# Kernel optimization log

Measured on AMD Instinct MI355X. Metric: run time of the kernel, lower is better.

## Reference

```python
import jax, jax.numpy as jnp
import numpy as np

N = 50000
E = 800000
IN_D, HID_D, EMB_D, K = 128, 128, 64, 16
ALPHA = 1.0
NEG_SLOPE = 0.2


def _l2norm(x, eps=1e-12):
    n = jnp.sqrt(jnp.sum(x * x, axis=1, keepdims=True))
    return x / jnp.maximum(n, eps)


def _gat(x, src, dst, W, a_src, a_dst, b, n_nodes):
    # PyG GATConv, heads=1: h = xW; e_ij = leakyrelu(a_src.h_j + a_dst.h_i)
    h = x @ W                                   # [N, D]
    al_s = h @ a_src                            # [N]
    al_d = h @ a_dst                            # [N]
    logits = jax.nn.leaky_relu(al_s[src] + al_d[dst], NEG_SLOPE)  # [E']
    m = jax.ops.segment_max(logits, dst, num_segments=n_nodes)
    ex = jnp.exp(logits - m[dst])
    denom = jax.ops.segment_sum(ex, dst, num_segments=n_nodes)
    alpha = ex / denom[dst]                     # softmax over incoming edges
    out = jax.ops.segment_sum(h[src] * alpha[:, None], dst, num_segments=n_nodes)
    return out + b


def _cluster_prob(z, cluster):
    z2 = jnp.sum(z * z, axis=1, keepdims=True)          # [N,1]
    c2 = jnp.sum(cluster * cluster, axis=1)[None, :]    # [1,K]
    dist = z2 + c2 - 2.0 * (z @ cluster.T)              # [N,K]
    q = 1.0 / (1.0 + dist / ALPHA)
    q = (q + 1e-07) ** ((ALPHA + 1.0) / 2.0)
    return q / jnp.sum(q, axis=1, keepdims=True)


def setup_inputs() -> dict:
    key = jax.random.key(0)
    ks = jax.random.split(key, 20)
    d = {}
    d['x'] = jax.random.normal(ks[0], (N, IN_D), dtype=jnp.float32)
    d['edge_index'] = jax.random.randint(ks[1], (2, E), 0, N, dtype=jnp.int32)
    dims = [(IN_D, HID_D), (HID_D, EMB_D), (EMB_D, HID_D), (HID_D, IN_D)]
    for i, (di, do) in enumerate(dims):
        s = 1.0 / np.sqrt(di)
        d[f'W{i+1}'] = jax.random.normal(ks[2 + 4 * i], (di, do), dtype=jnp.float32) * s
        d[f'a{i+1}s'] = jax.random.normal(ks[3 + 4 * i], (do,), dtype=jnp.float32) * 0.1
        d[f'a{i+1}d'] = jax.random.normal(ks[4 + 4 * i], (do,), dtype=jnp.float32) * 0.1
        d[f'b{i+1}'] = jnp.zeros((do,), dtype=jnp.float32)
    d['cluster'] = jax.random.normal(ks[18], (K, EMB_D), dtype=jnp.float32) * 0.1
    return d


def reference(x, edge_index, W1, a1s, a1d, b1, W2, a2s, a2d, b2,
              W3, a3s, a3d, b3, W4, a4s, a4d, b4, cluster):
    # add self loops (PyG GATConv default)
    loop = jnp.arange(N, dtype=edge_index.dtype)
    src = jnp.concatenate([edge_index[0], loop])
    dst = jnp.concatenate([edge_index[1], loop])

    xn = _l2norm(x)
    h1 = jax.nn.relu(_gat(xn, src, dst, W1, a1s, a1d, b1, N))
    z = _gat(h1, src, dst, W2, a2s, a2d, b2, N)
    z = _l2norm(z)
    d1 = jax.nn.relu(_gat(z, src, dst, W3, a3s, a3d, b3, N))
    x_hat = _gat(d1, src, dst, W4, a4s, a4d, b4, N)
    q = _cluster_prob(z, cluster)
    return (z, x_hat, q)
```

## Files before the change

### kernel.cpp

```cpp
#include <hip/hip_runtime.h>
#include <hip/hip_fp16.h>

#define NN 50000
#define NE 800000
#define NBK 196
#define BCAP 8192
#define GEMM_GRID 391
#define WTOT 49152

typedef unsigned int uint;
typedef unsigned short ushort;
typedef __attribute__((ext_vector_type(8))) short short8v;
typedef __attribute__((ext_vector_type(4))) float float4v;

static __device__ __forceinline__ float waveReduceSum(float v) {
#pragma unroll
  for (int o = 32; o > 0; o >>= 1) v += __shfl_xor(v, o);
  return v;
}
static __device__ __forceinline__ float waveReduceMax(float v) {
#pragma unroll
  for (int o = 32; o > 0; o >>= 1) v = fmaxf(v, __shfl_xor(v, o));
  return v;
}
static __device__ __forceinline__ uint f2bf(float f) {
  uint u = __float_as_uint(f);
  return (u + 0x7fffu + ((u >> 16) & 1u)) >> 16;
}
static __device__ __forceinline__ float h_lo(uint u) {
  __half2 h = *(const __half2*)&u;
  return __half2float(h.x);
}
static __device__ __forceinline__ float h_hi(uint u) {
  __half2 h = *(const __half2*)&u;
  return __half2float(h.y);
}
static __device__ __forceinline__ int waveInclScan(int v, int lane) {
#pragma unroll
  for (int o = 1; o < 64; o <<= 1) {
    int u = __shfl_up(v, o);
    if (lane >= o) v += u;
  }
  return v;
}
static __device__ __forceinline__ void split8(const float* f, short8v& hi, short8v& lo) {
#pragma unroll
  for (int j = 0; j < 8; ++j) {
    uint h = f2bf(f[j]);
    hi[j] = (short)h;
    float hf = __uint_as_float(h << 16);
    lo[j] = (short)f2bf(f[j] - hf);
  }
}

__global__ __launch_bounds__(256) void k_bucket(
    const int* __restrict__ esrc, const int* __restrict__ edst,
    uint* __restrict__ ebuf, int* __restrict__ bcnt) {
  __shared__ int hist[NBK];
  __shared__ int gbase[NBK];
  int tid = threadIdx.x;
  for (int i = tid; i < NBK; i += 256) hist[i] = 0;
  __syncthreads();
  const int ET = NE + NN;
  int base = blockIdx.x * 4096;
  int myb[16];
  uint mypk[16];
#pragma unroll
  for (int j = 0; j < 16; ++j) {
    int e = base + j * 256 + tid;
    int s, d;
    if (e < NE) { s = esrc[e]; d = edst[e]; }
    else if (e < ET) { s = e - NE; d = s; }
    else { myb[j] = -1; continue; }
    int b = d >> 8;
    myb[j] = b;
    mypk[j] = (uint)s | ((uint)(d & 255) << 16);
    atomicAdd(&hist[b], 1);
  }
  __syncthreads();
  for (int i = tid; i < NBK; i += 256) {
    int h = hist[i];
    gbase[i] = h > 0 ? atomicAdd(&bcnt[i], h) : 0;
    hist[i] = 0;
  }
  __syncthreads();
#pragma unroll
  for (int j = 0; j < 16; ++j) {
    int b = myb[j];
    if (b < 0) continue;
    int r = atomicAdd(&hist[b], 1);
    int pos = gbase[b] + r;
    if (pos < BCAP) ebuf[(size_t)b * BCAP + pos] = mypk[j];
  }
}
__global__ __launch_bounds__(256) void k_csr(
    const uint* __restrict__ ebuf, const int* __restrict__ bcnt,
    int* __restrict__ indptr, int* __restrict__ srcs) {
  __shared__ int h[256];
  __shared__ int cur[256];
  __shared__ int wsm[4];
  __shared__ int bbs;
  int tid = threadIdx.x, b = blockIdx.x;
  int lane = tid & 63, wv = tid >> 6;
  int v = (tid < NBK) ? bcnt[tid] : 0;
  int inc = waveInclScan(v, lane);
  if (lane == 63) wsm[wv] = inc;
  __syncthreads();
  int woff = 0;
  for (int k = 0; k < wv; ++k) woff += wsm[k];
  if (tid == b) bbs = inc - v + woff;
  h[tid] = 0;
  __syncthreads();
  int bbase = bbs;
  int cnt = bcnt[b];
  const uint* eb = ebuf + (size_t)b * BCAP;
  for (int i = tid; i < cnt; i += 256) atomicAdd(&h[eb[i] >> 16], 1);
  __syncthreads();
  int hv = h[tid];
  int inc2 = waveInclScan(hv, lane);
  if (lane == 63) wsm[wv] = inc2;
  __syncthreads();
  int woff2 = 0;
  for (int k = 0; k < wv; ++k) woff2 += wsm[k];
  int nodeExcl = inc2 - hv + woff2;
  int node = b * 256 + tid;
  if (node < NN) indptr[node] = bbase + nodeExcl;
  if (node == NN - 1) indptr[NN] = bbase + nodeExcl + hv;
  cur[tid] = nodeExcl;
  __syncthreads();
  for (int i = tid; i < cnt; i += 256) {
    uint pk = eb[i];
    int r = atomicAdd(&cur[pk >> 16], 1);
    srcs[bbase + r] = (int)(pk & 0xffffu);
  }
}

__global__ void k_wprep(const float* __restrict__ W1, const float* __restrict__ W2,
                        const float* __restrict__ W3, const float* __restrict__ W4,
                        ushort* __restrict__ hi, ushort* __restrict__ lo,
                        int* __restrict__ bcnt) {
  int i = blockIdx.x * 256 + threadIdx.x;
  if (i < NBK) bcnt[i] = 0;
  if (i >= WTOT) return;
  const float* W; int DO, base;
  if (i < 16384)      { W = W1; DO = 128; base = 0; }
  else if (i < 24576) { W = W2; DO = 64;  base = 16384; }
  else if (i < 32768) { W = W3; DO = 128; base = 24576; }
  else                { W = W4; DO = 128; base = 32768; }
  int idx = i - base;
  int k = idx / DO, col = idx % DO;
  float w = W[idx];
  uint h = f2bf(w);
  float hf = __uint_as_float(h << 16);
  uint l2 = f2bf(w - hf);
  int CT = DO >> 4;
  int fo = base + (((k >> 5) * CT + (col >> 4)) * 64 + ((col & 15) | (((k >> 3) & 3) << 4))) * 8 + (k & 7);
  hi[fo] = (ushort)h;
  lo[fo] = (ushort)l2;
}

template <int K, int DO, bool NORM>
__global__ __launch_bounds__(256) void k_gemm_mfma(
    const float* __restrict__ X, const ushort* __restrict__ Whi,
    const ushort* __restrict__ Wlo,
    const float* __restrict__ avs, const float* __restrict__ avd,
    ushort* __restrict__ H, float* __restrict__ als, float* __restrict__ ald, int n) {
  constexpr int KS = K / 32, CT = DO / 16;
  constexpr int W4N = K * DO / 8;
  __shared__ ushort sWhi[K * DO];
  __shared__ ushort sWlo[K * DO];
  __shared__ float sas[DO], sad[DO];
  int tid = threadIdx.x;
  for (int i = tid; i < DO; i += 256) { sas[i] = avs[i]; sad[i] = avd[i]; }
  {
    const uint4* ghi = (const uint4*)Whi;
    const uint4* glo = (const uint4*)Wlo;
    uint4* shi = (uint4*)sWhi;
    uint4* slo = (uint4*)sWlo;
    for (int i = tid; i < W4N; i += 256) { shi[i] = ghi[i]; slo[i] = glo[i]; }
  }
  __syncthreads();
  int lane = tid & 63, wv = tid >> 6;
  int ntiles = (n + 63) >> 6;
  for (int tile = blockIdx.x; tile < ntiles; tile += gridDim.x) {
    int r0 = tile * 64 + wv * 16;
    if (r0 >= n) continue;
    int row = r0 + (lane & 15);
    int sub = lane >> 4;
    const float* xrow = X + (size_t)row * K;
    float xr[KS][8];
#pragma unroll
    for (int s = 0; s < KS; ++s) {
      *(float4*)&xr[s][0] = *(const float4*)(xrow + s * 32 + sub * 8);
      *(float4*)&xr[s][4] = *(const float4*)(xrow + s * 32 + sub * 8 + 4);
    }
    if (NORM) {
      float ss = 0.f;
#pragma unroll
      for (int s = 0; s < KS; ++s)
#pragma unroll
        for (int j = 0; j < 8; ++j) ss += xr[s][j] * xr[s][j];
      ss += __shfl_xor(ss, 16);
      ss += __shfl_xor(ss, 32);
      float sc = 1.0f / fmaxf(sqrtf(ss), 1e-12f);
#pragma unroll
      for (int s = 0; s < KS; ++s)
#pragma unroll
        for (int j = 0; j < 8; ++j) xr[s][j] *= sc;
    }
    float4v acc[CT];
#pragma unroll
    for (int c = 0; c < CT; ++c) acc[c] = (float4v){0.f, 0.f, 0.f, 0.f};
#pragma unroll
    for (int s = 0; s < KS; ++s) {
      short8v ahi, alo;
      split8(xr[s], ahi, alo);
#pragma unroll
      for (int c = 0; c < CT; ++c) {
        short8v bhi = *(const short8v*)&sWhi[(s * CT + c) * 512 + lane * 8];
        short8v blo = *(const short8v*)&sWlo[(s * CT + c) * 512 + lane * 8];
        acc[c] = __builtin_amdgcn_mfma_f32_16x16x32_bf16(ahi, bhi, acc[c], 0, 0, 0);
        acc[c] = __builtin_amdgcn_mfma_f32_16x16x32_bf16(ahi, blo, acc[c], 0, 0, 0);
        acc[c] = __builtin_amdgcn_mfma_f32_16x16x32_bf16(alo, bhi, acc[c], 0, 0, 0);
      }
    }
    int rbase = r0 + (sub << 2);
    float alsp[4] = {0.f, 0.f, 0.f, 0.f};
    float aldp[4] = {0.f, 0.f, 0.f, 0.f};
#pragma unroll
    for (int c = 0; c < CT; ++c) {
      int col = (c << 4) + (lane & 15);
      float as_ = sas[col], ad_ = sad[col];
#pragma unroll
      for (int j = 0; j < 4; ++j) {
        float v = acc[c][j];
        alsp[j] += v * as_;
        aldp[j] += v * ad_;
        uint bv = (uint)__half_as_ushort(__float2half(v));
        uint nb = __shfl_xor(bv, 1);
        if (!(lane & 1)) {
          *(uint*)&H[(size_t)(rbase + j) * DO + col] = bv | (nb << 16);
        }
      }
    }
#pragma unroll
    for (int j = 0; j < 4; ++j) {
      float vs = alsp[j], vd = aldp[j];
#pragma unroll
      for (int o = 1; o < 16; o <<= 1) { vs += __shfl_xor(vs, o); vd += __shfl_xor(vd, o); }
      if ((lane & 15) == 0) { als[rbase + j] = vs; ald[rbase + j] = vd; }
    }
  }
}

template <int D, int MODE>
__global__ __launch_bounds__(256) void k_attn_aggr(
    const int* __restrict__ indptr, const int* __restrict__ srcs,
    const float* __restrict__ als, const float* __restrict__ ald,
    const ushort* __restrict__ H, const float* __restrict__ bias,
    float* __restrict__ out, const float* __restrict__ cluster,
    float* __restrict__ qout, int n) {
  constexpr int CAP = 256;
  __shared__ float slg[4][CAP];
  __shared__ int ssrc[4][CAP];
  __shared__ float scl[MODE == 2 ? 16 : 1][MODE == 2 ? 68 : 1];
  __shared__ float sz[4][MODE == 2 ? 64 : 4];
  int w = (blockIdx.x * blockDim.x + threadIdx.x) >> 6;
  int l = threadIdx.x & 63;
  int wv = threadIdx.x >> 6;
  if (MODE == 2) {
    for (int i = threadIdx.x; i < 1024; i += 256) scl[i >> 6][i & 63] = cluster[i];
    __syncthreads();
  }
  if (w >= n) return;
  int s0 = indptr[w], s1 = indptr[w + 1];
  int deg = s1 - s0;
  float ad = ald[w];
  float inv;
  float ax = 0.f, ay = 0.f, az = 0.f, aw = 0.f;
  const uint2* Hr = (const uint2*)H;
  if (deg <= CAP) {
    float mx = -1e30f;
    for (int t = l; t < deg; t += 64) {
      int s = srcs[s0 + t];
      float v = als[s] + ad;
      v = v >= 0.f ? v : 0.2f * v;
      ssrc[wv][t] = s;
      slg[wv][t] = v;
      mx = fmaxf(mx, v);
    }
    mx = waveReduceMax(mx);
    float sum = 0.f;
    for (int t = l; t < deg; t += 64) {
      float e = __expf(slg[wv][t] - mx);
      slg[wv][t] = e;
      sum += e;
    }
    sum = waveReduceSum(sum);
    inv = 1.0f / sum;
    if (D == 128) {
      int g = l >> 5, j = l & 31;
      int i = 0;
      for (; i + 16 <= deg; i += 16) {
        float p[8]; int e[8]; uint2 u[8];
#pragma unroll
        for (int r = 0; r < 8; ++r) { int idx = i + 2 * r + g; p[r] = slg[wv][idx]; e[r] = ssrc[wv][idx]; }
#pragma unroll
        for (int r = 0; r < 8; ++r) u[r] = Hr[(size_t)e[r] * 32 + j];
#pragma unroll
        for (int r = 0; r < 8; ++r) {
          ax += p[r] * h_lo(u[r].x); ay += p[r] * h_hi(u[r].x);
          az += p[r] * h_lo(u[r].y); aw += p[r] * h_hi(u[r].y);
        }
      }
      for (; i + 8 <= deg; i += 8) {
        float p[4]; int e[4]; uint2 u[4];
#pragma unroll
        for (int r = 0; r < 4; ++r) { int idx = i + 2 * r + g; p[r] = slg[wv][idx]; e[r] = ssrc[wv][idx]; }
#pragma unroll
        for (int r = 0; r < 4; ++r) u[r] = Hr[(size_t)e[r] * 32 + j];
#pragma unroll
        for (int r = 0; r < 4; ++r) {
          ax += p[r] * h_lo(u[r].x); ay += p[r] * h_hi(u[r].x);
          az += p[r] * h_lo(u[r].y); aw += p[r] * h_hi(u[r].y);
        }
      }
      for (; i < deg; i += 2) {
        int idx = i + g;
        if (idx < deg) {
          float p = slg[wv][idx];
          uint2 u = Hr[(size_t)ssrc[wv][idx] * 32 + j];
          ax += p * h_lo(u.x); ay += p * h_hi(u.x);
          az += p * h_lo(u.y); aw += p * h_hi(u.y);
        }
      }
    } else {
      int g = l >> 4, j = l & 15;
      int i = 0;
      for (; i + 32 <= deg; i += 32) {
        float p[8]; int e[8]; uint2 u[8];
#pragma unroll
        for (int r = 0; r < 8; ++r) { int idx = i + 4 * r + g; p[r] = slg[wv][idx]; e[r] = ssrc[wv][idx]; }
#pragma unroll
        for (int r = 0; r < 8; ++r) u[r] = Hr[(size_t)e[r] * 16 + j];
#pragma unroll
        for (int r = 0; r < 8; ++r) {
          ax += p[r] * h_lo(u[r].x); ay += p[r] * h_hi(u[r].x);
          az += p[r] * h_lo(u[r].y); aw += p[r] * h_hi(u[r].y);
        }
      }
      for (; i + 16 <= deg; i += 16) {
        float p[4]; int e[4]; uint2 u[4];
#pragma unroll
        for (int r = 0; r < 4; ++r) { int idx = i + 4 * r + g; p[r] = slg[wv][idx]; e[r] = ssrc[wv][idx]; }
#pragma unroll
        for (int r = 0; r < 4; ++r) u[r] = Hr[(size_t)e[r] * 16 + j];
#pragma unroll
        for (int r = 0; r < 4; ++r) {
          ax += p[r] * h_lo(u[r].x); ay += p[r] * h_hi(u[r].x);
          az += p[r] * h_lo(u[r].y); aw += p[r] * h_hi(u[r].y);
        }
      }
      for (; i < deg; i += 4) {
        int idx = i + g;
        if (idx < deg) {
          float p = slg[wv][idx];
          uint2 u = Hr[(size_t)ssrc[wv][idx] * 16 + j];
          ax += p * h_lo(u.x); ay += p * h_hi(u.x);
          az += p * h_lo(u.y); aw += p * h_hi(u.y);
        }
      }
    }
  } else {
    float mx = -1e30f;
    for (int t = l; t < deg; t += 64) {
      int s = srcs[s0 + t];
      float v = als[s] + ad;
      v = v >= 0.f ? v : 0.2f * v;
      mx = fmaxf(mx, v);
    }
    mx = waveReduceMax(mx);
    float sum = 0.f;
    for (int t = l; t < deg; t += 64) {
      int s = srcs[s0 + t];
      float v = als[s] + ad;
      v = v >= 0.f ? v : 0.2f * v;
      sum += __expf(v - mx);
    }
    sum = waveReduceSum(sum);
    inv = 1.0f / sum;
    for (int base = 0; base < deg; base += 64) {
      int t = base + l;
      if (t < deg) {
        int s = srcs[s0 + t];
        float v = als[s] + ad;
        v = v >= 0.f ? v : 0.2f * v;
        ssrc[wv][l] = s;
        slg[wv][l] = __expf(v - mx);
      }
      __builtin_amdgcn_wave_barrier();
      int m = min(64, deg - base);
      if (D == 128) {
        int g = l >> 5, j = l & 31;
        for (int i2 = g; i2 < m; i2 += 2) {
          float p = slg[wv][i2];
          uint2 u = Hr[(size_t)ssrc[wv][i2] * 32 + j];
          ax += p * h_lo(u.x); ay += p * h_hi(u.x);
          az += p * h_lo(u.y); aw += p * h_hi(u.y);
        }
      } else {
        int g = l >> 4, j = l & 15;
        for (int i2 = g; i2 < m; i2 += 4) {
          float p = slg[wv][i2];
          uint2 u = Hr[(size_t)ssrc[wv][i2] * 16 + j];
          ax += p * h_lo(u.x); ay += p * h_hi(u.x);
          az += p * h_lo(u.y); aw += p * h_hi(u.y);
        }
      }
      __builtin_amdgcn_wave_barrier();
    }
  }
  if (D == 128) {
    ax += __shfl_xor(ax, 32); ay += __shfl_xor(ay, 32);
    az += __shfl_xor(az, 32); aw += __shfl_xor(aw, 32);
    if (l < 32) {
      float4 bv = ((const float4*)bias)[l];
      float v0 = ax * inv + bv.x, v1 = ay * inv + bv.y;
      float v2 = az * inv + bv.z, v3 = aw * inv + bv.w;
      if (MODE == 1) {
        v0 = fmaxf(v0, 0.f); v1 = fmaxf(v1, 0.f);
        v2 = fmaxf(v2, 0.f); v3 = fmaxf(v3, 0.f);
      }
      ((float4*)(out + (size_t)w * 128))[l] = make_float4(v0, v1, v2, v3);
    }
  } else {
    ax += __shfl_xor(ax, 16); ay += __shfl_xor(ay, 16);
    az += __shfl_xor(az, 16); aw += __shfl_xor(aw, 16);
    ax += __shfl_xor(ax, 32); ay += __shfl_xor(ay, 32);
    az += __shfl_xor(az, 32); aw += __shfl_xor(aw, 32);
    int j = l & 15;
    float4 bv = ((const float4*)bias)[j];
    float v0 = ax * inv + bv.x, v1 = ay * inv + bv.y;
    float v2 = az * inv + bv.z, v3 = aw * inv + bv.w;
    if (MODE == 2) {
      float ss = v0 * v0 + v1 * v1 + v2 * v2 + v3 * v3;
      ss += __shfl_xor(ss, 1); ss += __shfl_xor(ss, 2);
      ss += __shfl_xor(ss, 4); ss += __shfl_xor(ss, 8);
      float sc = 1.0f / fmaxf(sqrtf(ss), 1e-12f);
      v0 *= sc; v1 *= sc; v2 *= sc; v3 *= sc;
    }
    if (l < 16) ((float4*)(out + (size_t)w * 64))[j] = make_float4(v0, v1, v2, v3);
    if (MODE == 2) {
      if (l < 16) ((float4*)&sz[wv][0])[j] = make_float4(v0, v1, v2, v3);
      __builtin_amdgcn_wave_barrier();
      int kk = l >> 2, p = l & 3;
      const float* zr = &sz[wv][p * 16];
      const float* cr = &scl[kk][p * 16];
      float s = 0.f;
#pragma unroll
      for (int d = 0; d < 16; ++d) {
        float df = zr[d] - cr[d];
        s += df * df;
      }
      s += __shfl_xor(s, 1);
      s += __shfl_xor(s, 2);
      float qv = 1.0f / (1.0f + s) + 1e-7f;
      float t = qv;
      t += __shfl_xor(t, 4);
      t += __shfl_xor(t, 8);
      t += __shfl_xor(t, 16);
      t += __shfl_xor(t, 32);
      if (p == 0) qout[(size_t)w * 16 + kk] = qv / t;
    }
  }
}

extern "C" void kernel_launch(void* const* d_in, const int* in_sizes, int n_in,
                              void* d_out, int out_size, void* d_ws, size_t ws_size,
                              hipStream_t stream) {
  const float* x = (const float*)d_in[0];
  const int* ei = (const int*)d_in[1];
  const float* W1 = (const float*)d_in[2];
  const float* a1s = (const float*)d_in[3];
  const float* a1d = (const float*)d_in[4];
  const float* b1 = (const float*)d_in[5];
  const float* W2 = (const float*)d_in[6];
  const float* a2s = (const float*)d_in[7];
  const float* a2d = (const float*)d_in[8];
  const float* b2 = (const float*)d_in[9];
  const float* W3 = (const float*)d_in[10];
  const float* a3s = (const float*)d_in[11];
  const float* a3d = (const float*)d_in[12];
  const float* b3 = (const float*)d_in[13];
  const float* W4 = (const float*)d_in[14];
  const float* a4s = (const float*)d_in[15];
  const float* a4d = (const float*)d_in[16];
  const float* b4 = (const float*)d_in[17];
  const float* cluster = (const float*)d_in[18];

  float* out = (float*)d_out;
  float* z = out;
  float* xhat = out + (size_t)NN * 64;
  float* qout = xhat + (size_t)NN * 128;

  const int ET = NE + NN;
  float* wsf = (float*)d_ws;
  float* X = wsf;          wsf += (size_t)NN * 128;
  ushort* H = (ushort*)wsf; wsf += (size_t)NN * 64;
  float* als = wsf;        wsf += NN;
  float* ald = wsf;        wsf += NN;
  int* indptr = (int*)wsf; wsf += NN + 1;
  int* srcs = (int*)wsf;   wsf += ET;
  uint* ebuf = (uint*)wsf; wsf += (size_t)NBK * BCAP;
  int* bcnt = (int*)wsf;   wsf += NBK;
  ushort* wfhi = (ushort*)wsf; wsf += WTOT / 2;
  ushort* wflo = (ushort*)wsf; wsf += WTOT / 2;

  const int* esrc = ei;
  const int* edst = ei + NE;

  const int TB = 256;
  const int gW = (NN + 3) / 4;
  const int gB = (ET + 4095) / 4096;

  k_wprep<<<(WTOT + 255) / 256, 256, 0, stream>>>(W1, W2, W3, W4, wfhi, wflo, bcnt);
  k_bucket<<<gB, 256, 0, stream>>>(esrc, edst, ebuf, bcnt);
  k_csr<<<NBK, 256, 0, stream>>>(ebuf, bcnt, indptr, srcs);

  k_gemm_mfma<128, 128, true><<<GEMM_GRID, 256, 0, stream>>>(
      x, wfhi, wflo, a1s, a1d, H, als, ald, NN);
  k_attn_aggr<128, 1><<<gW, TB, 0, stream>>>(indptr, srcs, als, ald, H, b1, X,
                                             nullptr, nullptr, NN);

  k_gemm_mfma<128, 64, false><<<GEMM_GRID, 256, 0, stream>>>(
      X, wfhi + 16384, wflo + 16384, a2s, a2d, H, als, ald, NN);
  k_attn_aggr<64, 2><<<gW, TB, 0, stream>>>(indptr, srcs, als, ald, H, b2, z,
                                            cluster, qout, NN);

  k_gemm_mfma<64, 128, false><<<GEMM_GRID, 256, 0, stream>>>(
      z, wfhi + 24576, wflo + 24576, a3s, a3d, H, als, ald, NN);
  k_attn_aggr<128, 1><<<gW, TB, 0, stream>>>(indptr, srcs, als, ald, H, b3, X,
                                             nullptr, nullptr, NN);

  k_gemm_mfma<128, 128, false><<<GEMM_GRID, 256, 0, stream>>>(
      X, wfhi + 32768, wflo + 32768, a4s, a4d, H, als, ald, NN);
  k_attn_aggr<128, 0><<<gW, TB, 0, stream>>>(indptr, srcs, als, ald, H, b4, xhat,
                                             nullptr, nullptr, NN);
}
```

Baseline: 244.9 us.

## Split each node's edge aggregation across two waves with shared-memory reduction

The attention aggregation kernel now assigns two waves per destination node, each handling half of the incoming edges. The softmax max and sum and the partial feature accumulators are combined through shared memory with block barriers. Source offsets are prescaled by the row stride, and the unrolled gather loops become predicated fixed-width loops. The aim is more memory-level parallelism for the random row gathers, at the cost of extra block synchronisation and fewer edges per wave.

```diff
diff --git a/kernel.cpp b/kernel.cpp
--- a/kernel.cpp
+++ b/kernel.cpp
@@ -261,165 +261,135 @@
     float* __restrict__ out, const float* __restrict__ cluster,
     float* __restrict__ qout, int n) {
   constexpr int CAP = 256;
-  __shared__ float slg[4][CAP];
-  __shared__ int ssrc[4][CAP];
+  constexpr int HSTR = D / 4;
+  __shared__ float slg[2][CAP];
+  __shared__ uint soff[2][CAP];
+  __shared__ float wredm[4], wreds[4];
+  __shared__ float pacc[2][64][5];
   __shared__ float scl[MODE == 2 ? 16 : 1][MODE == 2 ? 68 : 1];
-  __shared__ float sz[4][MODE == 2 ? 64 : 4];
-  int w = (blockIdx.x * blockDim.x + threadIdx.x) >> 6;
-  int l = threadIdx.x & 63;
-  int wv = threadIdx.x >> 6;
+  __shared__ float sz[2][MODE == 2 ? 64 : 1];
+  int tid = threadIdx.x;
+  int l = tid & 63;
+  int wv = tid >> 6;
+  int nd = wv >> 1, q = wv & 1;
   if (MODE == 2) {
-    for (int i = threadIdx.x; i < 1024; i += 256) scl[i >> 6][i & 63] = cluster[i];
-    __syncthreads();
-  }
-  if (w >= n) return;
-  int s0 = indptr[w], s1 = indptr[w + 1];
-  int deg = s1 - s0;
-  float ad = ald[w];
-  float inv;
-  float ax = 0.f, ay = 0.f, az = 0.f, aw = 0.f;
+    for (int i = tid; i < 1024; i += 256) scl[i >> 6][i & 63] = cluster[i];
+  }
+  int w = blockIdx.x * 2 + nd;
+  bool act = (w < n);
+  int s0 = 0, deg = 0;
+  float ad = 0.f;
+  if (act) { s0 = indptr[w]; deg = indptr[w + 1] - s0; ad = ald[w]; }
+  bool staged = act && (deg <= CAP);
+  int h1 = (deg + 1) >> 1;
+  int myS = q ? h1 : 0;
+  int myE = q ? deg : h1;
   const uint2* Hr = (const uint2*)H;
-  if (deg <= CAP) {
-    float mx = -1e30f;
-    for (int t = l; t < deg; t += 64) {
-      int s = srcs[s0 + t];
-      float v = als[s] + ad;
-      v = v >= 0.f ? v : 0.2f * v;
-      ssrc[wv][t] = s;
-      slg[wv][t] = v;
-      mx = fmaxf(mx, v);
-    }
-    mx = waveReduceMax(mx);
-    float sum = 0.f;
-    for (int t = l; t < deg; t += 64) {
-      float e = __expf(slg[wv][t] - mx);
-      slg[wv][t] = e;
+  float mx = -1e30f;
+  for (int t = myS + l; t < myE; t += 64) {
+    int s = srcs[s0 + t];
+    float v = als[s] + ad;
+    v = v >= 0.f ? v : 0.2f * v;
+    if (staged) { slg[nd][t] = v; soff[nd][t] = (uint)s * HSTR; }
+    mx = fmaxf(mx, v);
+  }
+  mx = waveReduceMax(mx);
+  if (l == 0) wredm[wv] = mx;
+  __syncthreads();
+  mx = fmaxf(wredm[nd * 2], wredm[nd * 2 + 1]);
+  float sum = 0.f;
+  if (staged) {
+    for (int t = myS + l; t < myE; t += 64) {
+      float e = __expf(slg[nd][t] - mx);
+      slg[nd][t] = e;
       sum += e;
     }
-    sum = waveReduceSum(sum);
-    inv = 1.0f / sum;
-    if (D == 128) {
-      int g = l >> 5, j = l & 31;
-      int i = 0;
-      for (; i + 16 <= deg; i += 16) {
-        float p[8]; int e[8]; uint2 u[8];
-#pragma unroll
-        for (int r = 0; r < 8; ++r) { int idx = i + 2 * r + g; p[r] = slg[wv][idx]; e[r] = ssrc[wv][idx]; }
-#pragma unroll
-        for (int r = 0; r < 8; ++r) u[r] = Hr[(size_t)e[r] * 32 + j];
-#pragma unroll
-        for (int r = 0; r < 8; ++r) {
-          ax += p[r] * h_lo(u[r].x); ay += p[r] * h_hi(u[r].x);
-          az += p[r] * h_lo(u[r].y); aw += p[r] * h_hi(u[r].y);
-        }
-      }
-      for (; i + 8 <= deg; i += 8) {
-        float p[4]; int e[4]; uint2 u[4];
-#pragma unroll
-        for (int r = 0; r < 4; ++r) { int idx = i + 2 * r + g; p[r] = slg[wv][idx]; e[r] = ssrc[wv][idx]; }
-#pragma unroll
-        for (int r = 0; r < 4; ++r) u[r] = Hr[(size_t)e[r] * 32 + j];
-#pragma unroll
-        for (int r = 0; r < 4; ++r) {
-          ax += p[r] * h_lo(u[r].x); ay += p[r] * h_hi(u[r].x);
-          az += p[r] * h_lo(u[r].y); aw += p[r] * h_hi(u[r].y);
-        }
-      }
-      for (; i < deg; i += 2) {
-        int idx = i + g;
-        if (idx < deg) {
-          float p = slg[wv][idx];
-          uint2 u = Hr[(size_t)ssrc[wv][idx] * 32 + j];
-          ax += p * h_lo(u.x); ay += p * h_hi(u.x);
-          az += p * h_lo(u.y); aw += p * h_hi(u.y);
-        }
-      }
-    } else {
-      int g = l >> 4, j = l & 15;
-      int i = 0;
-      for (; i + 32 <= deg; i += 32) {
-        float p[8]; int e[8]; uint2 u[8];
-#pragma unroll
-        for (int r = 0; r < 8; ++r) { int idx = i + 4 * r + g; p[r] = slg[wv][idx]; e[r] = ssrc[wv][idx]; }
-#pragma unroll
-        for (int r = 0; r < 8; ++r) u[r] = Hr[(size_t)e[r] * 16 + j];
-#pragma unroll
-        for (int r = 0; r < 8; ++r) {
-          ax += p[r] * h_lo(u[r].x); ay += p[r] * h_hi(u[r].x);
-          az += p[r] * h_lo(u[r].y); aw += p[r] * h_hi(u[r].y);
-        }
-      }
-      for (; i + 16 <= deg; i += 16) {
-        float p[4]; int e[4]; uint2 u[4];
-#pragma unroll
-        for (int r = 0; r < 4; ++r) { int idx = i + 4 * r + g; p[r] = slg[wv][idx]; e[r] = ssrc[wv][idx]; }
-#pragma unroll
-        for (int r = 0; r < 4; ++r) u[r] = Hr[(size_t)e[r] * 16 + j];
-#pragma unroll
-        for (int r = 0; r < 4; ++r) {
-          ax += p[r] * h_lo(u[r].x); ay += p[r] * h_hi(u[r].x);
-          az += p[r] * h_lo(u[r].y); aw += p[r] * h_hi(u[r].y);
-        }
-      }
-      for (; i < deg; i += 4) {
-        int idx = i + g;
-        if (idx < deg) {
-          float p = slg[wv][idx];
-          uint2 u = Hr[(size_t)ssrc[wv][idx] * 16 + j];
-          ax += p * h_lo(u.x); ay += p * h_hi(u.x);
-          az += p * h_lo(u.y); aw += p * h_hi(u.y);
-        }
-      }
-    }
-  } else {
-    float mx = -1e30f;
-    for (int t = l; t < deg; t += 64) {
-      int s = srcs[s0 + t];
-      float v = als[s] + ad;
-      v = v >= 0.f ? v : 0.2f * v;
-      mx = fmaxf(mx, v);
-    }
-    mx = waveReduceMax(mx);
-    float sum = 0.f;
-    for (int t = l; t < deg; t += 64) {
+  } else if (act) {
+    for (int t = myS + l; t < myE; t += 64) {
       int s = srcs[s0 + t];
       float v = als[s] + ad;
       v = v >= 0.f ? v : 0.2f * v;
       sum += __expf(v - mx);
     }
-    sum = waveReduceSum(sum);
-    inv = 1.0f / sum;
-    for (int base = 0; base < deg; base += 64) {
-      int t = base + l;
-      if (t < deg) {
-        int s = srcs[s0 + t];
+  }
+  sum = waveReduceSum(sum);
+  if (l == 0) wreds[wv] = sum;
+  __syncthreads();
+  float inv = act ? 1.0f / (wreds[nd * 2] + wreds[nd * 2 + 1]) : 0.f;
+  float ax = 0.f, ay = 0.f, az = 0.f, aw = 0.f;
+  if (staged) {
+    if (D == 128) {
+      int g = l >> 5, j = l & 31;
+      for (int i = myS; i < myE; i += 16) {
+        int c8 = min((myE - i - g + 1) >> 1, 8);
+        float p[8]; uint of[8]; uint2 u[8];
+#pragma unroll
+        for (int r = 0; r < 8; ++r) if (r < c8) {
+          int idx = i + 2 * r + g;
+          p[r] = slg[nd][idx];
+          of[r] = soff[nd][idx];
+        }
+#pragma unroll
+        for (int r = 0; r < 8; ++r) if (r < c8) u[r] = Hr[(size_t)of[r] + j];
+#pragma unroll
+        for (int r = 0; r < 8; ++r) if (r < c8) {
+          ax += p[r] * h_lo(u[r].x); ay += p[r] * h_hi(u[r].x);
+          az += p[r] * h_lo(u[r].y); aw += p[r] * h_hi(u[r].y);
+        }
+      }
+    } else {
+      int g = l >> 4, j = l & 15;
+      for (int i = myS; i < myE; i += 16) {
+        int c4 = min((myE - i - g + 3) >> 2, 4);
+        float p[4]; uint of[4]; uint2 u[4];
+#pragma unroll
+        for (int r = 0; r < 4; ++r) if (r < c4) {
+          int idx = i + 4 * r + g;
+          p[r] = slg[nd][idx];
+          of[r] = soff[nd][idx];
+        }
+#pragma unroll
+        for (int r = 0; r < 4; ++r) if (r < c4) u[r] = Hr[(size_t)of[r] + j];
+#pragma unroll
+        for (int r = 0; r < 4; ++r) if (r < c4) {
+          ax += p[r] * h_lo(u[r].x); ay += p[r] * h_hi(u[r].x);
+          az += p[r] * h_lo(u[r].y); aw += p[r] * h_hi(u[r].y);
+        }
+      }
+    }
+  } else if (act) {
+    if (D == 128) {
+      int g = l >> 5, j = l & 31;
+      for (int idx = myS + g; idx < myE; idx += 2) {
+        int s = srcs[s0 + idx];
         float v = als[s] + ad;
         v = v >= 0.f ? v : 0.2f * v;
-        ssrc[wv][l] = s;
-        slg[wv][l] = __expf(v - mx);
-      }
-      __builtin_amdgcn_wave_barrier();
-      int m = min(64, deg - base);
-      if (D == 128) {
-        int g = l >> 5, j = l & 31;
-        for (int i2 = g; i2 < m; i2 += 2) {
-          float p = slg[wv][i2];
-          uint2 u = Hr[(size_t)ssrc[wv][i2] * 32 + j];
-          ax += p * h_lo(u.x); ay += p * h_hi(u.x);
-          az += p * h_lo(u.y); aw += p * h_hi(u.y);
-        }
-      } else {
-        int g = l >> 4, j = l & 15;
-        for (int i2 = g; i2 < m; i2 += 4) {
-          float p = slg[wv][i2];
-          uint2 u = Hr[(size_t)ssrc[wv][i2] * 16 + j];
-          ax += p * h_lo(u.x); ay += p * h_hi(u.x);
-          az += p * h_lo(u.y); aw += p * h_hi(u.y);
-        }
-      }
-      __builtin_amdgcn_wave_barrier();
-    }
-  }
+        float p = __expf(v - mx);
+        uint2 u = Hr[(size_t)s * HSTR + j];
+        ax += p * h_lo(u.x); ay += p * h_hi(u.x);
+        az += p * h_lo(u.y); aw += p * h_hi(u.y);
+      }
+    } else {
+      int g = l >> 4, j = l & 15;
+      for (int idx = myS + g; idx < myE; idx += 4) {
+        int s = srcs[s0 + idx];
+        float v = als[s] + ad;
+        v = v >= 0.f ? v : 0.2f * v;
+        float p = __expf(v - mx);
+        uint2 u = Hr[(size_t)s * HSTR + j];
+        ax += p * h_lo(u.x); ay += p * h_hi(u.x);
+        az += p * h_lo(u.y); aw += p * h_hi(u.y);
+      }
+    }
+  }
+  if (q == 1) {
+    pacc[nd][l][0] = ax; pacc[nd][l][1] = ay;
+    pacc[nd][l][2] = az; pacc[nd][l][3] = aw;
+  }
+  __syncthreads();
+  if (q == 1 || !act) return;
+  ax += pacc[nd][l][0]; ay += pacc[nd][l][1];
+  az += pacc[nd][l][2]; aw += pacc[nd][l][3];
   if (D == 128) {
     ax += __shfl_xor(ax, 32); ay += __shfl_xor(ay, 32);
     az += __shfl_xor(az, 32); aw += __shfl_xor(aw, 32);
@@ -451,10 +421,10 @@
     }
     if (l < 16) ((float4*)(out + (size_t)w * 64))[j] = make_float4(v0, v1, v2, v3);
     if (MODE == 2) {
-      if (l < 16) ((float4*)&sz[wv][0])[j] = make_float4(v0, v1, v2, v3);
+      if (l < 16) ((float4*)&sz[nd][0])[j] = make_float4(v0, v1, v2, v3);
       __builtin_amdgcn_wave_barrier();
       int kk = l >> 2, p = l & 3;
-      const float* zr = &sz[wv][p * 16];
+      const float* zr = &sz[nd][p * 16];
       const float* cr = &scl[kk][p * 16];
       float s = 0.f;
 #pragma unroll
@@ -520,7 +490,7 @@
   const int* edst = ei + NE;
 
   const int TB = 256;
-  const int gW = (NN + 3) / 4;
+  const int gA = (NN + 1) / 2;
   const int gB = (ET + 4095) / 4096;
 
   k_wprep<<<(WTOT + 255) / 256, 256, 0, stream>>>(W1, W2, W3, W4, wfhi, wflo, bcnt);
@@ -529,21 +499,21 @@
 
   k_gemm_mfma<128, 128, true><<<GEMM_GRID, 256, 0, stream>>>(
       x, wfhi, wflo, a1s, a1d, H, als, ald, NN);
-  k_attn_aggr<128, 1><<<gW, TB, 0, stream>>>(indptr, srcs, als, ald, H, b1, X,
+  k_attn_aggr<128, 1><<<gA, TB, 0, stream>>>(indptr, srcs, als, ald, H, b1, X,
                                              nullptr, nullptr, NN);
 
   k_gemm_mfma<128, 64, false><<<GEMM_GRID, 256, 0, stream>>>(
       X, wfhi + 16384, wflo + 16384, a2s, a2d, H, als, ald, NN);
-  k_attn_aggr<64, 2><<<gW, TB, 0, stream>>>(indptr, srcs, als, ald, H, b2, z,
+  k_attn_aggr<64, 2><<<gA, TB, 0, stream>>>(indptr, srcs, als, ald, H, b2, z,
                                             cluster, qout, NN);
 
   k_gemm_mfma<64, 128, false><<<GEMM_GRID, 256, 0, stream>>>(
       z, wfhi + 24576, wflo + 24576, a3s, a3d, H, als, ald, NN);
-  k_attn_aggr<128, 1><<<gW, TB, 0, stream>>>(indptr, srcs, als, ald, H, b3, X,
+  k_attn_aggr<128, 1><<<gA, TB, 0, stream>>>(indptr, srcs, als, ald, H, b3, X,
                                              nullptr, nullptr, NN);
 
   k_gemm_mfma<128, 128, false><<<GEMM_GRID, 256, 0, stream>>>(
       X, wfhi + 32768, wflo + 32768, a4s, a4d, H, als, ald, NN);
-  k_attn_aggr<128, 0><<<gW, TB, 0, stream>>>(indptr, srcs, als, ald, H, b4, xhat,
+  k_attn_aggr<128, 0><<<gA, TB, 0, stream>>>(indptr, srcs, als, ald, H, b4, xhat,
                                              nullptr, nullptr, NN);
 }
```

After: 350.5 us. +43.1%, slower.
